# Kernel optimization log

Measured on AMD Instinct MI355X. Metric: run time of the kernel, lower is better.

## Reference

```python
import jax, jax.numpy as jnp
import numpy as np

NUM_SEGMENTS = 4096  # number of episodes (len(batch['lengths']))


def setup_inputs() -> dict:
    key = jax.random.key(0)
    k1, k2, k3, k4, k5 = jax.random.split(key, 5)
    N = 65536
    emb_a = jax.random.normal(k1, (N, 256), dtype=jnp.float32)
    emb_b = jax.random.normal(k2, (N, 256), dtype=jnp.float32)
    segment_ids = jnp.sort(jax.random.randint(k3, (N,), 0, NUM_SEGMENTS, dtype=jnp.int32))
    W = jax.random.normal(k4, (32, 512), dtype=jnp.float32) * (1.0 / np.sqrt(512.0))
    b = jax.random.normal(k5, (32,), dtype=jnp.float32) * 0.01
    return {"emb_a": emb_a, "emb_b": emb_b, "segment_ids": segment_ids, "W": W, "b": b}


def reference(emb_a, emb_b, segment_ids, W, b):
    # torch.cat([embeds[key] for key in project_keys], dim=1)
    combined = jnp.concatenate([emb_a, emb_b], axis=1)  # [N, 512]
    # split_with_sizes + per-split mean + stack == segment mean
    sums = jax.ops.segment_sum(combined, segment_ids, num_segments=NUM_SEGMENTS)  # [S, 512]
    counts = jax.ops.segment_sum(jnp.ones((combined.shape[0],), combined.dtype),
                                 segment_ids, num_segments=NUM_SEGMENTS)  # [S]
    pooled = sums / jnp.maximum(counts, 1.0)[:, None]  # [S, 512]
    # dropout is identity in eval mode; final nn.Linear
    return pooled @ W.T + b  # [S, 32]
```

## Files before the change

kernel.cpp:

```cpp
#include <hip/hip_runtime.h>

#define NSEG 4096

__global__ __launch_bounds__(256) void scatter_bounds_kernel(
    const int* __restrict__ seg, int* __restrict__ bounds, int nrows)
{
    const int i = blockIdx.x * 256 + threadIdx.x;
    if (i >= nrows) return;
    const int cur  = seg[i];
    const int prev = (i == 0) ? -1 : seg[i - 1];
    for (int s = prev + 1; s <= cur; ++s) bounds[s] = i;
    if (i == nrows - 1) {
        for (int s = cur + 1; s <= NSEG; ++s) bounds[s] = nrows;
    }
}

__global__ __launch_bounds__(256, 4) void fused_pool_proj_kernel(
    const float* __restrict__ emb_a,
    const float* __restrict__ emb_b,
    const int*   __restrict__ bounds,
    const float* __restrict__ W,
    const float* __restrict__ bias,
    float*       __restrict__ out)
{
    const int s    = blockIdx.x;
    const int t    = threadIdx.x;
    const int wave = t >> 6;
    const int lane = t & 63;

    __shared__ float pooled[1024];
    __shared__ float sh_out[32];

    const int start = bounds[s];
    const int end   = bounds[s + 1];
    const int cnt   = end - start;
    const int mid   = start + (cnt >> 1);

    const int r0 = (wave >> 1) ? mid : start;
    const int r1 = (wave >> 1) ? end : mid;

    const float*  base = (wave & 1) ? emb_b : emb_a;
    const float4* src  = reinterpret_cast<const float4*>(base) + lane;

    float4 a0 = make_float4(0.f,0.f,0.f,0.f);
    float4 a1 = make_float4(0.f,0.f,0.f,0.f);
    float4 a2 = make_float4(0.f,0.f,0.f,0.f);
    float4 a3 = make_float4(0.f,0.f,0.f,0.f);

    int r = r0;
    for (; r + 4 <= r1; r += 4) {
        float4 v0 = src[(size_t)(r + 0) * 64];
        float4 v1 = src[(size_t)(r + 1) * 64];
        float4 v2 = src[(size_t)(r + 2) * 64];
        float4 v3 = src[(size_t)(r + 3) * 64];
        a0.x += v0.x; a0.y += v0.y; a0.z += v0.z; a0.w += v0.w;
        a1.x += v1.x; a1.y += v1.y; a1.z += v1.z; a1.w += v1.w;
        a2.x += v2.x; a2.y += v2.y; a2.z += v2.z; a2.w += v2.w;
        a3.x += v3.x; a3.y += v3.y; a3.z += v3.z; a3.w += v3.w;
    }
    for (; r < r1; ++r) {
        float4 v = src[(size_t)r * 64];
        a0.x += v.x; a0.y += v.y; a0.z += v.z; a0.w += v.w;
    }

    float4 acc;
    acc.x = a0.x + a1.x + a2.x + a3.x;
    acc.y = a0.y + a1.y + a2.y + a3.y;
    acc.z = a0.z + a1.z + a2.z + a3.z;
    acc.w = a0.w + a1.w + a2.w + a3.w;

    *reinterpret_cast<float4*>(pooled + (wave << 8) + (lane << 2)) = acc;
    __syncthreads();

    const float inv = 1.0f / (float)max(cnt, 1);
    const float4* pool4 = reinterpret_cast<const float4*>(pooled);
    const float4 qa0 = pool4[lane];
    const float4 qa1 = pool4[128 + lane];
    const float4 qb0 = pool4[64 + lane];
    const float4 qb1 = pool4[192 + lane];
    float4 p0, p1;
    p0.x = (qa0.x + qa1.x) * inv;  p0.y = (qa0.y + qa1.y) * inv;
    p0.z = (qa0.z + qa1.z) * inv;  p0.w = (qa0.w + qa1.w) * inv;
    p1.x = (qb0.x + qb1.x) * inv;  p1.y = (qb0.y + qb1.y) * inv;
    p1.z = (qb0.z + qb1.z) * inv;  p1.w = (qb0.w + qb1.w) * inv;

    #pragma unroll 4
    for (int jj = 0; jj < 8; ++jj) {
        const int j = (wave << 3) + jj;
        const float4* wrow = reinterpret_cast<const float4*>(W + j * 512);
        const float4  w0 = wrow[lane];
        const float4  w1 = wrow[64 + lane];
        float v = p0.x*w0.x + p0.y*w0.y + p0.z*w0.z + p0.w*w0.w
                + p1.x*w1.x + p1.y*w1.y + p1.z*w1.z + p1.w*w1.w;
        v += __shfl_xor(v, 1);
        v += __shfl_xor(v, 2);
        v += __shfl_xor(v, 4);
        v += __shfl_xor(v, 8);
        v += __shfl_xor(v, 16);
        v += __shfl_xor(v, 32);
        if (lane == 0) sh_out[j] = v + bias[j];
    }
    __syncthreads();

    if (t < 32) out[s * 32 + t] = sh_out[t];
}

__global__ __launch_bounds__(128, 8) void fused_fallback_kernel(
    const float* __restrict__ emb_a,
    const float* __restrict__ emb_b,
    const int*   __restrict__ seg,
    const float* __restrict__ W,
    const float* __restrict__ bias,
    float*       __restrict__ out,
    int nrows)
{
    const int s = blockIdx.x;
    const int t = threadIdx.x;
    const int wave = t >> 6;
    const int lane = t & 63;
    __shared__ int   bounds[2];
    __shared__ float pooled[512];
    __shared__ float sh_out[32];
    if (t < 2) {
        int target = s + t;
        int lo = 0, hi = nrows;
        while (lo < hi) { int mid = (lo + hi) >> 1; if (seg[mid] < target) lo = mid + 1; else hi = mid; }
        bounds[t] = lo;
    }
    __syncthreads();
    const int start = bounds[0], end = bounds[1];
    const int cnt = end - start;
    const float*  base = (wave == 0) ? emb_a : emb_b;
    const float4* src  = reinterpret_cast<const float4*>(base) + lane;
    float4 a0 = make_float4(0.f,0.f,0.f,0.f);
    float4 a1 = make_float4(0.f,0.f,0.f,0.f);
    float4 a2 = make_float4(0.f,0.f,0.f,0.f);
    float4 a3 = make_float4(0.f,0.f,0.f,0.f);
    int r = start;
    for (; r + 4 <= end; r += 4) {
        float4 v0 = src[(size_t)(r + 0) * 64];
        float4 v1 = src[(size_t)(r + 1) * 64];
        float4 v2 = src[(size_t)(r + 2) * 64];
        float4 v3 = src[(size_t)(r + 3) * 64];
        a0.x += v0.x; a0.y += v0.y; a0.z += v0.z; a0.w += v0.w;
        a1.x += v1.x; a1.y += v1.y; a1.z += v1.z; a1.w += v1.w;
        a2.x += v2.x; a2.y += v2.y; a2.z += v2.z; a2.w += v2.w;
        a3.x += v3.x; a3.y += v3.y; a3.z += v3.z; a3.w += v3.w;
    }
    for (; r < end; ++r) {
        float4 v = src[(size_t)r * 64];
        a0.x += v.x; a0.y += v.y; a0.z += v.z; a0.w += v.w;
    }
    const float inv = 1.0f / (float)max(cnt, 1);
    float4 acc;
    acc.x = (a0.x + a1.x + a2.x + a3.x) * inv;
    acc.y = (a0.y + a1.y + a2.y + a3.y) * inv;
    acc.z = (a0.z + a1.z + a2.z + a3.z) * inv;
    acc.w = (a0.w + a1.w + a2.w + a3.w) * inv;
    *reinterpret_cast<float4*>(pooled + (wave << 8) + (lane << 2)) = acc;
    __syncthreads();
    const float4* pool4 = reinterpret_cast<const float4*>(pooled);
    const float4  p0 = pool4[lane];
    const float4  p1 = pool4[64 + lane];
    #pragma unroll 4
    for (int jj = 0; jj < 16; ++jj) {
        const int j = (wave << 4) + jj;
        const float4* wrow = reinterpret_cast<const float4*>(W + j * 512);
        const float4  w0 = wrow[lane];
        const float4  w1 = wrow[64 + lane];
        float v = p0.x*w0.x + p0.y*w0.y + p0.z*w0.z + p0.w*w0.w
                + p1.x*w1.x + p1.y*w1.y + p1.z*w1.z + p1.w*w1.w;
        v += __shfl_xor(v, 1);
        v += __shfl_xor(v, 2);
        v += __shfl_xor(v, 4);
        v += __shfl_xor(v, 8);
        v += __shfl_xor(v, 16);
        v += __shfl_xor(v, 32);
        if (lane == 0) sh_out[j] = v + bias[j];
    }
    __syncthreads();
    if (t < 32) out[s * 32 + t] = sh_out[t];
}

extern "C" void kernel_launch(void* const* d_in, const int* in_sizes, int n_in,
                              void* d_out, int out_size, void* d_ws, size_t ws_size,
                              hipStream_t stream) {
    const float* emb_a = (const float*)d_in[0];
    const float* emb_b = (const float*)d_in[1];
    const int*   seg   = (const int*)d_in[2];
    const float* W     = (const float*)d_in[3];
    const float* bias  = (const float*)d_in[4];
    float*       out   = (float*)d_out;
    const int nrows = in_sizes[2];

    const size_t need = (size_t)(NSEG + 1) * sizeof(int);
    if (ws_size >= need) {
        int* bounds = (int*)d_ws;
        scatter_bounds_kernel<<<(nrows + 255) / 256, 256, 0, stream>>>(seg, bounds, nrows);
        fused_pool_proj_kernel<<<NSEG, 256, 0, stream>>>(emb_a, emb_b, bounds, W, bias, out);
    } else {
        fused_fallback_kernel<<<NSEG, 128, 0, stream>>>(emb_a, emb_b, seg, W, bias, out, nrows);
    }
}
```

Before: 38.10 us.

## Use persistent work-stealing blocks with atomic ticket for segment pooling

Replaces the one-block-per-segment launch with 2048 persistent blocks that claim further segments through an atomic ticket counter, which the setup kernel resets. The aim is to cut block launch and scheduling overhead and to balance uneven segment sizes. It also raises the occupancy hint to 8 blocks per CU and unrolls the row accumulation by 8 to keep more loads in flight. In exchange it adds an atomic and an extra barrier for every segment, and the grid is close to the number of resident slots, so the dynamic scheduling gains little.

```diff
diff --git a/kernel.cpp b/kernel.cpp
--- a/kernel.cpp
+++ b/kernel.cpp
@@ -1,11 +1,20 @@
 #include <hip/hip_runtime.h>
 
-#define NSEG 4096
-
-__global__ __launch_bounds__(256) void scatter_bounds_kernel(
-    const int* __restrict__ seg, int* __restrict__ bounds, int nrows)
+#define NSEG    4096
+#define NBLOCKS 2048
+
+__device__ __forceinline__ void acc4(float4& a, const float4 v) {
+    a.x += v.x; a.y += v.y; a.z += v.z; a.w += v.w;
+}
+
+__global__ __launch_bounds__(256) void setup_kernel(
+    const int* __restrict__ seg,
+    int*       __restrict__ ticket,
+    int*       __restrict__ bounds,
+    int nrows)
 {
     const int i = blockIdx.x * 256 + threadIdx.x;
+    if (i == 0) *ticket = 0;
     if (i >= nrows) return;
     const int cur  = seg[i];
     const int prev = (i == 0) ? -1 : seg[i - 1];
@@ -15,94 +24,104 @@
     }
 }
 
-__global__ __launch_bounds__(256, 4) void fused_pool_proj_kernel(
+__global__ __launch_bounds__(256, 8) void fused_ws_kernel(
     const float* __restrict__ emb_a,
     const float* __restrict__ emb_b,
     const int*   __restrict__ bounds,
     const float* __restrict__ W,
     const float* __restrict__ bias,
+    int*         __restrict__ ticket,
     float*       __restrict__ out)
 {
-    const int s    = blockIdx.x;
     const int t    = threadIdx.x;
     const int wave = t >> 6;
     const int lane = t & 63;
 
     __shared__ float pooled[1024];
     __shared__ float sh_out[32];
-
-    const int start = bounds[s];
-    const int end   = bounds[s + 1];
-    const int cnt   = end - start;
-    const int mid   = start + (cnt >> 1);
-
-    const int r0 = (wave >> 1) ? mid : start;
-    const int r1 = (wave >> 1) ? end : mid;
+    __shared__ int   sh_s;
 
     const float*  base = (wave & 1) ? emb_b : emb_a;
     const float4* src  = reinterpret_cast<const float4*>(base) + lane;
 
-    float4 a0 = make_float4(0.f,0.f,0.f,0.f);
-    float4 a1 = make_float4(0.f,0.f,0.f,0.f);
-    float4 a2 = make_float4(0.f,0.f,0.f,0.f);
-    float4 a3 = make_float4(0.f,0.f,0.f,0.f);
-
-    int r = r0;
-    for (; r + 4 <= r1; r += 4) {
-        float4 v0 = src[(size_t)(r + 0) * 64];
-        float4 v1 = src[(size_t)(r + 1) * 64];
-        float4 v2 = src[(size_t)(r + 2) * 64];
-        float4 v3 = src[(size_t)(r + 3) * 64];
-        a0.x += v0.x; a0.y += v0.y; a0.z += v0.z; a0.w += v0.w;
-        a1.x += v1.x; a1.y += v1.y; a1.z += v1.z; a1.w += v1.w;
-        a2.x += v2.x; a2.y += v2.y; a2.z += v2.z; a2.w += v2.w;
-        a3.x += v3.x; a3.y += v3.y; a3.z += v3.z; a3.w += v3.w;
-    }
-    for (; r < r1; ++r) {
-        float4 v = src[(size_t)r * 64];
-        a0.x += v.x; a0.y += v.y; a0.z += v.z; a0.w += v.w;
-    }
-
-    float4 acc;
-    acc.x = a0.x + a1.x + a2.x + a3.x;
-    acc.y = a0.y + a1.y + a2.y + a3.y;
-    acc.z = a0.z + a1.z + a2.z + a3.z;
-    acc.w = a0.w + a1.w + a2.w + a3.w;
-
-    *reinterpret_cast<float4*>(pooled + (wave << 8) + (lane << 2)) = acc;
-    __syncthreads();
-
-    const float inv = 1.0f / (float)max(cnt, 1);
-    const float4* pool4 = reinterpret_cast<const float4*>(pooled);
-    const float4 qa0 = pool4[lane];
-    const float4 qa1 = pool4[128 + lane];
-    const float4 qb0 = pool4[64 + lane];
-    const float4 qb1 = pool4[192 + lane];
-    float4 p0, p1;
-    p0.x = (qa0.x + qa1.x) * inv;  p0.y = (qa0.y + qa1.y) * inv;
-    p0.z = (qa0.z + qa1.z) * inv;  p0.w = (qa0.w + qa1.w) * inv;
-    p1.x = (qb0.x + qb1.x) * inv;  p1.y = (qb0.y + qb1.y) * inv;
-    p1.z = (qb0.z + qb1.z) * inv;  p1.w = (qb0.w + qb1.w) * inv;
-
-    #pragma unroll 4
-    for (int jj = 0; jj < 8; ++jj) {
-        const int j = (wave << 3) + jj;
-        const float4* wrow = reinterpret_cast<const float4*>(W + j * 512);
-        const float4  w0 = wrow[lane];
-        const float4  w1 = wrow[64 + lane];
-        float v = p0.x*w0.x + p0.y*w0.y + p0.z*w0.z + p0.w*w0.w
-                + p1.x*w1.x + p1.y*w1.y + p1.z*w1.z + p1.w*w1.w;
-        v += __shfl_xor(v, 1);
-        v += __shfl_xor(v, 2);
-        v += __shfl_xor(v, 4);
-        v += __shfl_xor(v, 8);
-        v += __shfl_xor(v, 16);
-        v += __shfl_xor(v, 32);
-        if (lane == 0) sh_out[j] = v + bias[j];
-    }
-    __syncthreads();
-
-    if (t < 32) out[s * 32 + t] = sh_out[t];
+    int s = blockIdx.x;
+
+    for (;;) {
+        const int start = bounds[s];
+        const int end   = bounds[s + 1];
+        const int cnt   = end - start;
+        const int mid   = start + (cnt >> 1);
+        const int r0    = (wave >> 1) ? mid : start;
+        const int r1    = (wave >> 1) ? end : mid;
+
+        float4 a0{0,0,0,0}, a1{0,0,0,0}, a2{0,0,0,0}, a3{0,0,0,0};
+        int r = r0;
+        for (; r + 8 <= r1; r += 8) {
+            float4 v0 = src[(size_t)(r+0)*64];
+            float4 v1 = src[(size_t)(r+1)*64];
+            float4 v2 = src[(size_t)(r+2)*64];
+            float4 v3 = src[(size_t)(r+3)*64];
+            float4 v4 = src[(size_t)(r+4)*64];
+            float4 v5 = src[(size_t)(r+5)*64];
+            float4 v6 = src[(size_t)(r+6)*64];
+            float4 v7 = src[(size_t)(r+7)*64];
+            acc4(a0, v0); acc4(a1, v1); acc4(a2, v2); acc4(a3, v3);
+            acc4(a0, v4); acc4(a1, v5); acc4(a2, v6); acc4(a3, v7);
+        }
+        for (; r + 4 <= r1; r += 4) {
+            float4 v0 = src[(size_t)(r+0)*64];
+            float4 v1 = src[(size_t)(r+1)*64];
+            float4 v2 = src[(size_t)(r+2)*64];
+            float4 v3 = src[(size_t)(r+3)*64];
+            acc4(a0, v0); acc4(a1, v1); acc4(a2, v2); acc4(a3, v3);
+        }
+        for (; r < r1; ++r) acc4(a0, src[(size_t)r * 64]);
+
+        float4 acc;
+        acc.x = a0.x + a1.x + a2.x + a3.x;
+        acc.y = a0.y + a1.y + a2.y + a3.y;
+        acc.z = a0.z + a1.z + a2.z + a3.z;
+        acc.w = a0.w + a1.w + a2.w + a3.w;
+        *reinterpret_cast<float4*>(pooled + (wave << 8) + (lane << 2)) = acc;
+        __syncthreads();
+
+        const float inv = 1.0f / (float)max(cnt, 1);
+        const float4* pool4 = reinterpret_cast<const float4*>(pooled);
+        const float4 qa0 = pool4[lane];
+        const float4 qb0 = pool4[64 + lane];
+        const float4 qa1 = pool4[128 + lane];
+        const float4 qb1 = pool4[192 + lane];
+        float4 p0, p1;
+        p0.x = (qa0.x + qa1.x) * inv;  p0.y = (qa0.y + qa1.y) * inv;
+        p0.z = (qa0.z + qa1.z) * inv;  p0.w = (qa0.w + qa1.w) * inv;
+        p1.x = (qb0.x + qb1.x) * inv;  p1.y = (qb0.y + qb1.y) * inv;
+        p1.z = (qb0.z + qb1.z) * inv;  p1.w = (qb0.w + qb1.w) * inv;
+
+        #pragma unroll 4
+        for (int jj = 0; jj < 8; ++jj) {
+            const int j = (wave << 3) + jj;
+            const float4* wrow = reinterpret_cast<const float4*>(W + j * 512);
+            const float4  w0 = wrow[lane];
+            const float4  w1 = wrow[64 + lane];
+            float v = p0.x*w0.x + p0.y*w0.y + p0.z*w0.z + p0.w*w0.w
+                    + p1.x*w1.x + p1.y*w1.y + p1.z*w1.z + p1.w*w1.w;
+            v += __shfl_xor(v, 1);
+            v += __shfl_xor(v, 2);
+            v += __shfl_xor(v, 4);
+            v += __shfl_xor(v, 8);
+            v += __shfl_xor(v, 16);
+            v += __shfl_xor(v, 32);
+            if (lane == 0) sh_out[j] = v + bias[j];
+        }
+        __syncthreads();
+
+        if (t < 32) out[s * 32 + t] = sh_out[t];
+
+        if (t == 0) sh_s = NBLOCKS + atomicAdd(ticket, 1);
+        __syncthreads();
+        s = sh_s;
+        if (s >= NSEG) break;
+    }
 }
 
 __global__ __launch_bounds__(128, 8) void fused_fallback_kernel(
@@ -118,39 +137,30 @@
     const int t = threadIdx.x;
     const int wave = t >> 6;
     const int lane = t & 63;
-    __shared__ int   bounds[2];
+    __shared__ int   bnd[2];
     __shared__ float pooled[512];
     __shared__ float sh_out[32];
     if (t < 2) {
         int target = s + t;
         int lo = 0, hi = nrows;
         while (lo < hi) { int mid = (lo + hi) >> 1; if (seg[mid] < target) lo = mid + 1; else hi = mid; }
-        bounds[t] = lo;
+        bnd[t] = lo;
     }
     __syncthreads();
-    const int start = bounds[0], end = bounds[1];
+    const int start = bnd[0], end = bnd[1];
     const int cnt = end - start;
     const float*  base = (wave == 0) ? emb_a : emb_b;
     const float4* src  = reinterpret_cast<const float4*>(base) + lane;
-    float4 a0 = make_float4(0.f,0.f,0.f,0.f);
-    float4 a1 = make_float4(0.f,0.f,0.f,0.f);
-    float4 a2 = make_float4(0.f,0.f,0.f,0.f);
-    float4 a3 = make_float4(0.f,0.f,0.f,0.f);
+    float4 a0{0,0,0,0}, a1{0,0,0,0}, a2{0,0,0,0}, a3{0,0,0,0};
     int r = start;
     for (; r + 4 <= end; r += 4) {
-        float4 v0 = src[(size_t)(r + 0) * 64];
-        float4 v1 = src[(size_t)(r + 1) * 64];
-        float4 v2 = src[(size_t)(r + 2) * 64];
-        float4 v3 = src[(size_t)(r + 3) * 64];
-        a0.x += v0.x; a0.y += v0.y; a0.z += v0.z; a0.w += v0.w;
-        a1.x += v1.x; a1.y += v1.y; a1.z += v1.z; a1.w += v1.w;
-        a2.x += v2.x; a2.y += v2.y; a2.z += v2.z; a2.w += v2.w;
-        a3.x += v3.x; a3.y += v3.y; a3.z += v3.z; a3.w += v3.w;
-    }
-    for (; r < end; ++r) {
-        float4 v = src[(size_t)r * 64];
-        a0.x += v.x; a0.y += v.y; a0.z += v.z; a0.w += v.w;
-    }
+        float4 v0 = src[(size_t)(r+0)*64];
+        float4 v1 = src[(size_t)(r+1)*64];
+        float4 v2 = src[(size_t)(r+2)*64];
+        float4 v3 = src[(size_t)(r+3)*64];
+        acc4(a0, v0); acc4(a1, v1); acc4(a2, v2); acc4(a3, v3);
+    }
+    for (; r < end; ++r) acc4(a0, src[(size_t)r * 64]);
     const float inv = 1.0f / (float)max(cnt, 1);
     float4 acc;
     acc.x = (a0.x + a1.x + a2.x + a3.x) * inv;
@@ -193,11 +203,12 @@
     float*       out   = (float*)d_out;
     const int nrows = in_sizes[2];
 
-    const size_t need = (size_t)(NSEG + 1) * sizeof(int);
+    const size_t need = 64 + (size_t)(NSEG + 1) * sizeof(int);
     if (ws_size >= need) {
-        int* bounds = (int*)d_ws;
-        scatter_bounds_kernel<<<(nrows + 255) / 256, 256, 0, stream>>>(seg, bounds, nrows);
-        fused_pool_proj_kernel<<<NSEG, 256, 0, stream>>>(emb_a, emb_b, bounds, W, bias, out);
+        int* ticket = (int*)d_ws;
+        int* bounds = (int*)((char*)d_ws + 64);
+        setup_kernel<<<(nrows + 255) / 256, 256, 0, stream>>>(seg, ticket, bounds, nrows);
+        fused_ws_kernel<<<NBLOCKS, 256, 0, stream>>>(emb_a, emb_b, bounds, W, bias, ticket, out);
     } else {
         fused_fallback_kernel<<<NSEG, 128, 0, stream>>>(emb_a, emb_b, seg, W, bias, out, nrows);
     }
```

Result: slower. 76.69 us (+101.3%).
